# Performance work log

Hardware: AMD Instinct MI355X
Metric: run time of the kernel (lower is better)

## Reference

```python
import jax, jax.numpy as jnp
import numpy as np

B, N, NC = 16, 25200, 80
CONF_THRES = 0.25
IOU_THRES = 0.45
MAX_DET = 300
MAX_WH = 7680.0   # yolov5 per-class box offset for class-aware NMS
TOPK = 1024       # pre-NMS candidate cap (fixed-shape stand-in for yolov5 max_nms)


def setup_inputs():
    key = jax.random.key(0)
    k1, k2 = jax.random.split(key)
    # xywh in pixel units (640x640 image, boxes up to ~120 px); obj/cls confidences in [0,1]
    xywh = jax.random.uniform(k1, (B, N, 4), dtype=jnp.float32) * jnp.array([640.0, 640.0, 120.0, 120.0], jnp.float32)
    conf = jax.random.uniform(k2, (B, N, 1 + NC), dtype=jnp.float32)
    return {"YOLOoutput": jnp.concatenate([xywh, conf], axis=-1)}


def _xywh2xyxy(x):
    cx, cy, w, h = x[..., 0], x[..., 1], x[..., 2], x[..., 3]
    return jnp.stack([cx - w / 2, cy - h / 2, cx + w / 2, cy + h / 2], axis=-1)


def _pairwise_iou(a, b):
    # a, b: [K,4] xyxy -> [K,K]
    lt = jnp.maximum(a[:, None, :2], b[None, :, :2])
    rb = jnp.minimum(a[:, None, 2:], b[None, :, 2:])
    wh = jnp.maximum(rb - lt, 0.0)
    inter = wh[..., 0] * wh[..., 1]
    area_a = (a[:, 2] - a[:, 0]) * (a[:, 3] - a[:, 1])
    area_b = (b[:, 2] - b[:, 0]) * (b[:, 3] - b[:, 1])
    return inter / (area_a[:, None] + area_b[None, :] - inter + 1e-7)


def _nms_single(pred):
    # pred: [N, 5+NC]
    obj = pred[:, 4]
    cls_conf = pred[:, 5:] * obj[:, None]      # conf = obj_conf * cls_conf (yolov5)
    conf = jnp.max(cls_conf, axis=-1)
    j = jnp.argmax(cls_conf, axis=-1)
    valid = (obj > CONF_THRES) & (conf > CONF_THRES)
    box = _xywh2xyxy(pred[:, :4])
    scores = jnp.where(valid, conf, -1.0)      # invalid candidates sink to bottom
    top_scores, idx = jax.lax.top_k(scores, TOPK)
    b = box[idx]                               # [TOPK,4]
    c = j[idx].astype(box.dtype)
    boxes_off = b + (c * MAX_WH)[:, None]      # class-aware NMS via per-class offset
    valid_k = top_scores > 0.0
    iou = _pairwise_iou(boxes_off, boxes_off)
    ar = jnp.arange(TOPK)

    def body(i, supp):
        active = jnp.logical_not(supp[i])
        return supp | (active & (iou[i] > IOU_THRES) & (ar > i))

    supp = jax.lax.fori_loop(0, TOPK, body, jnp.logical_not(valid_k))
    keep = valid_k & jnp.logical_not(supp)
    fs, fi = jax.lax.top_k(jnp.where(keep, top_scores, -1.0), MAX_DET)
    dv = fs > 0.0
    det_box = b[fi] * dv[:, None]              # zero out padded rows
    det = jnp.concatenate(
        [det_box, jnp.where(dv, fs, 0.0)[:, None], (c[fi] * dv)[:, None]], axis=-1
    )                                          # [MAX_DET, 6] = x1,y1,x2,y2,conf,cls
    return det, dv


def reference(YOLOoutput):
    det, dvalid = jax.vmap(_nms_single)(YOLOoutput)   # [B,MAX_DET,6], [B,MAX_DET]
    scores = det[..., 4]
    mean_conf = jnp.max(scores, axis=1)               # = 0 when image has no detections
    n = dvalid.sum(axis=1)
    terms = jnp.abs(det[..., 0:2] - det[..., 2:4]) * scores[..., None]  # padded rows are 0
    s = terms.sum(axis=(1, 2))
    wh = jnp.where(n > 0, s / (2.0 * jnp.maximum(n, 1)), 0.0)  # mean over n*2 elements
    conf_addition = mean_conf.sum() / B
    w_and_h = wh.sum() / B
    return conf_addition, w_and_h, det[2]
```

## Files before the change

kernel.cpp:

```cpp
#include <hip/hip_runtime.h>
#include <hip/hip_bf16.h>

typedef unsigned long long u64;
typedef unsigned int u32;

#define BATCH 16
#define NANCH 25200
#define NCLS 80
#define NFEAT 85
#define TOPK 1024
#define MAXDET 300
#define CONF_T 0.25f
#define IOU_T 0.45f
#define MAX_WH 7680.0f

#define TILE_A 128
#define TILES_PER_BLK 4

__global__ __launch_bounds__(512) void score_kernel(const float* __restrict__ in,
                                                    u64* __restrict__ keys) {
    __shared__ float ld[TILE_A * NFEAT];
    const int b = blockIdx.y, tid = threadIdx.x;
    for (int t = 0; t < TILES_PER_BLK; ++t) {
        const int tile = blockIdx.x * TILES_PER_BLK + t;
        const int a0 = tile * TILE_A;
        if (a0 >= NANCH) break;
        const int na = min(TILE_A, NANCH - a0);
        const int nf4 = na * NFEAT / 4;
        const float4* src = (const float4*)(in + ((size_t)b * NANCH + a0) * NFEAT);
        if (t) __syncthreads();
        for (int k = tid; k < nf4; k += 512) ((float4*)ld)[k] = src[k];
        __syncthreads();
        const int a = tid >> 2, q = tid & 3;
        if (a < na) {
            const float* p = ld + a * NFEAT;
            float obj = p[4];
            float best = -1e30f;
            int bj = 0;
#pragma unroll
            for (int k = 0; k < 20; ++k) {
                float v = p[5 + q * 20 + k] * obj;
                if (v > best) { best = v; bj = q * 20 + k; }
            }
#pragma unroll
            for (int d = 1; d < 4; d <<= 1) {
                float ob = __shfl_xor(best, d, 64);
                int oj = __shfl_xor(bj, d, 64);
                if (ob > best || (ob == best && oj < bj)) { best = ob; bj = oj; }
            }
            if (q == 0) {
                bool valid = (obj > CONF_T) && (best > CONF_T);
                float sc = valid ? best : -1.0f;
                u32 sb = __float_as_uint(sc);
                u32 ord = sb ^ ((sb & 0x80000000u) ? 0xFFFFFFFFu : 0x80000000u);
                int idx = a0 + a;
                keys[(size_t)b * NANCH + idx] =
                    ((u64)ord << 32) | ((u64)((u32)(idx ^ 0xFFFF) & 0xFFFFu) << 8) | (u64)bj;
            }
        }
    }
}

__global__ __launch_bounds__(1024) void select_topk(const u64* __restrict__ keys,
                                                    const float* __restrict__ in,
                                                    float4* __restrict__ box4,
                                                    float4* __restrict__ boxoff4,
                                                    float* __restrict__ score,
                                                    float* __restrict__ cls,
                                                    u64* __restrict__ vmask) {
    const int b = blockIdx.x, tid = threadIdx.x;
    const u64* kb = keys + (size_t)b * NANCH;
    __shared__ u32 hist[256];
    __shared__ u32 sfx[256];
    __shared__ u32 s_prefix, s_cg, s_cnt;
    __shared__ u64 buf[2048];

    if (tid == 0) { s_prefix = 0u; s_cg = 0u; }
    for (int p = 0; p < 4; ++p) {
        if (tid < 256) hist[tid] = 0u;
        __syncthreads();
        const u32 prefix = s_prefix;
        const u32 cg = s_cg;
        const int sh_match = 32 - 8 * p;
        const int sh_dig = 24 - 8 * p;
#pragma unroll 4
        for (int n = tid; n < NANCH; n += 1024) {
            u32 hi = (u32)(kb[n] >> 32);
            if (((u64)(hi ^ prefix) >> sh_match) == 0ull)
                atomicAdd(&hist[(hi >> sh_dig) & 0xFFu], 1u);
        }
        __syncthreads();
        if (tid < 256) sfx[tid] = hist[tid];
        __syncthreads();
        for (int off = 1; off < 256; off <<= 1) {
            u32 v = 0u;
            if (tid < 256 && tid + off < 256) v = sfx[tid + off];
            __syncthreads();
            if (tid < 256) sfx[tid] += v;
            __syncthreads();
        }
        const u32 need = (u32)TOPK - cg;
        if (tid < 256) {
            u32 s0 = sfx[tid];
            u32 s1 = (tid < 255) ? sfx[tid + 1] : 0u;
            if (s0 >= need && s1 < need) {
                s_prefix = prefix | ((u32)tid << sh_dig);
                s_cg = cg + s1;
            }
        }
        __syncthreads();
    }
    const u32 thr = s_prefix;
    if (tid == 0) s_cnt = 0u;
    __syncthreads();
#pragma unroll 4
    for (int n = tid; n < NANCH; n += 1024) {
        u64 k = kb[n];
        if ((u32)(k >> 32) > thr) {
            u32 pos = atomicAdd(&s_cnt, 1u);
            if (pos < 2048u) buf[pos] = k;
        }
    }
    __syncthreads();
#pragma unroll 4
    for (int n = tid; n < NANCH; n += 1024) {
        u64 k = kb[n];
        if ((u32)(k >> 32) == thr) {
            u32 pos = atomicAdd(&s_cnt, 1u);
            if (pos < 2048u) buf[pos] = k;
        }
    }
    __syncthreads();
    u32 cnt = s_cnt; if (cnt > 2048u) cnt = 2048u;
    for (int n = (int)cnt + tid; n < 2048; n += 1024) buf[n] = 0ull;
    __syncthreads();
    for (int k2 = 2; k2 <= 2048; k2 <<= 1) {
        for (int jj = k2 >> 1; jj > 0; jj >>= 1) {
            int i = ((tid & ~(jj - 1)) << 1) | (tid & (jj - 1));
            int part = i | jj;
            u64 a = buf[i], c = buf[part];
            bool sw = ((i & k2) == 0) ? (a < c) : (a > c);
            if (sw) { buf[i] = c; buf[part] = a; }
            __syncthreads();
        }
    }
    u64 k = buf[tid];
    u32 ord = (u32)(k >> 32);
    u32 sb = (ord & 0x80000000u) ? (ord ^ 0x80000000u) : ~ord;
    float sc = __uint_as_float(sb);
    int idx = (int)((((u32)(k >> 8)) & 0xFFFFu) ^ 0xFFFFu);
    int j = (int)(k & 0xFFu);
    const float* pr = in + ((size_t)b * NANCH + idx) * NFEAT;
    float cx = pr[0], cy = pr[1], ww = pr[2], hh = pr[3];
    float x1 = cx - ww / 2.0f, y1 = cy - hh / 2.0f;
    float x2 = cx + ww / 2.0f, y2 = cy + hh / 2.0f;
    float c = (float)j;
    float cm = c * MAX_WH;
    box4[b * TOPK + tid]    = make_float4(x1, y1, x2, y2);
    boxoff4[b * TOPK + tid] = make_float4(x1 + cm, y1 + cm, x2 + cm, y2 + cm);
    score[b * TOPK + tid] = sc;
    cls[b * TOPK + tid] = c;
    u64 bal = __ballot(sc > 0.0f);
    if ((tid & 63) == 0) vmask[b * 16 + (tid >> 6)] = bal;
}

__global__ __launch_bounds__(256) void iou_mask(const float4* __restrict__ boxoff4,
                                                u64* __restrict__ M) {
    const int wavei = (blockIdx.x << 2) | (threadIdx.x >> 6);
    const int lane = threadIdx.x & 63;
    const int b = wavei >> 10;
    const int i = wavei & 1023;
    const float4 A = boxoff4[b * TOPK + i];
    const float areaA = (A.z - A.x) * (A.w - A.y);
    u64 myword = 0ull;
#pragma unroll 4
    for (int t = 0; t < 16; ++t) {
        int j = (t << 6) | lane;
        float4 Bx = boxoff4[b * TOPK + j];
        float lx = fmaxf(A.x, Bx.x), ly = fmaxf(A.y, Bx.y);
        float rx = fminf(A.z, Bx.z), ry = fminf(A.w, Bx.w);
        float iw = fmaxf(rx - lx, 0.0f), ih = fmaxf(ry - ly, 0.0f);
        float inter = iw * ih;
        float areaB = (Bx.z - Bx.x) * (Bx.w - Bx.y);
        float iou = inter / (areaA + areaB - inter + 1e-7f);
        bool pred = (iou > IOU_T) && (j > i);
        u64 bal = __ballot(pred);
        if (lane == t) myword = bal;
    }
    if (lane < 16) M[((size_t)b * 16 + lane) * TOPK + i] = myword;
}

__global__ __launch_bounds__(64) void nms_seq(const u64* __restrict__ M,
                                              const u64* __restrict__ vmask,
                                              u64* __restrict__ keepmask) {
    const int lane = threadIdx.x;
    const int b = blockIdx.x * 4 + (lane >> 4);
    const int w = lane & 15;
    u64 supp = ~vmask[b * 16 + w];
    const u64* Mw = M + ((size_t)b * 16 + w) * TOPK;
    const u64* Mbase = M + (size_t)b * 16 * TOPK;
    for (int wb = 0; wb < 16; ++wb) {
        u64 cur = __shfl(supp, (lane & 48) | wb, 64);
        const u64* Mc = Mbase + (size_t)wb * TOPK;
        u64 rw[8], rc[8], nw[8], nc[8];
#pragma unroll
        for (int q = 0; q < 8; ++q) { rw[q] = Mw[wb * 64 + q]; rc[q] = Mc[wb * 64 + q]; }
        for (int cblk = 0; cblk < 8; ++cblk) {
            if (cblk < 7) {
                const int i0n = wb * 64 + (cblk + 1) * 8;
#pragma unroll
                for (int q = 0; q < 8; ++q) { nw[q] = Mw[i0n + q]; nc[q] = Mc[i0n + q]; }
            }
#pragma unroll
            for (int q = 0; q < 8; ++q) {
                int ii = cblk * 8 + q;
                u64 msk = ((cur >> ii) & 1ull) ? 0ull : ~0ull;
                supp |= rw[q] & msk;
                cur  |= rc[q] & msk;
            }
#pragma unroll
            for (int q = 0; q < 8; ++q) { rw[q] = nw[q]; rc[q] = nc[q]; }
        }
    }
    keepmask[b * 16 + w] = vmask[b * 16 + w] & ~supp;
}

__global__ __launch_bounds__(256) void finalize(const float4* __restrict__ box4,
                                                const float* __restrict__ score,
                                                const float* __restrict__ cls,
                                                const u64* __restrict__ keepmask,
                                                float* __restrict__ out) {
    const int b = blockIdx.x, tid = threadIdx.x;
    __shared__ u64 kw[16];
    __shared__ int wpfx[17];
    __shared__ float sdet[MAXDET * 6];
    __shared__ float s_sum, s_max;
    if (tid < 16) kw[tid] = keepmask[b * 16 + tid];
    if (tid == 0) { s_sum = 0.0f; s_max = 0.0f; }
    __syncthreads();
    if (tid == 0) {
        int acc = 0;
        for (int w = 0; w < 16; ++w) { wpfx[w] = acc; acc += __popcll(kw[w]); }
        wpfx[16] = acc;
    }
    for (int t = tid; t < MAXDET * 6; t += 256) sdet[t] = 0.0f;
    __syncthreads();
    for (int r = tid; r < TOPK; r += 256) {
        int w = r >> 6, bp = r & 63;
        if ((kw[w] >> bp) & 1ull) {
            int pos = wpfx[w] + __popcll(kw[w] & ((1ull << bp) - 1ull));
            if (pos < MAXDET) {
                float4 bx = box4[b * TOPK + r];
                float s = score[b * TOPK + r];
                float c = cls[b * TOPK + r];
                sdet[pos * 6 + 0] = bx.x;
                sdet[pos * 6 + 1] = bx.y;
                sdet[pos * 6 + 2] = bx.z;
                sdet[pos * 6 + 3] = bx.w;
                sdet[pos * 6 + 4] = s;
                sdet[pos * 6 + 5] = c;
                float term = (fabsf(bx.x - bx.z) + fabsf(bx.y - bx.w)) * s;
                atomicAdd(&s_sum, term);
                if (pos == 0) s_max = s;
            }
        }
    }
    __syncthreads();
    if (tid == 0) {
        int n = wpfx[16]; if (n > MAXDET) n = MAXDET;
        float wh = (n > 0) ? (s_sum / (2.0f * (float)n)) : 0.0f;
        atomicAdd(&out[0], s_max / (float)BATCH);
        atomicAdd(&out[1], wh / (float)BATCH);
    }
    if (b == 2) {
        for (int t = tid; t < MAXDET * 6; t += 256) out[2 + t] = sdet[t];
    }
}

extern "C" void kernel_launch(void* const* d_in, const int* in_sizes, int n_in,
                              void* d_out, int out_size, void* d_ws, size_t ws_size,
                              hipStream_t stream) {
    const float* in = (const float*)d_in[0];
    float* out = (float*)d_out;
    char* ws = (char*)d_ws;

    u64*    keys     = (u64*)   (ws + 0);
    float4* boxoff4  = (float4*)(ws + 3225600);
    float4* box4     = (float4*)(ws + 3225600 + 262144);
    float*  score    = (float*) (ws + 3749888);
    float*  cls      = (float*) (ws + 3815424);
    u64*    vmask    = (u64*)   (ws + 3880960);
    u64*    M        = (u64*)   (ws + 3883008);
    u64*    keepmask = (u64*)   (ws + 5980160);

    hipMemsetAsync(out, 0, 2 * sizeof(float), stream);
    score_kernel<<<dim3(50, BATCH), 512, 0, stream>>>(in, keys);
    select_topk<<<BATCH, 1024, 0, stream>>>(keys, in, box4, boxoff4, score, cls, vmask);
    iou_mask<<<BATCH * TOPK / 4, 256, 0, stream>>>(boxoff4, M);
    nms_seq<<<4, 64, 0, stream>>>(M, vmask, keepmask);
    finalize<<<BATCH, 256, 0, stream>>>(box4, score, cls, keepmask, out);
}
```

Before: 341.2 us.

## Use wave shuffles for histogram scan, bitonic sort stages, and transpose NMS mask

The histogram suffix scan in top-k selection becomes a single-wave shuffle scan instead of a barrier-heavy shared-memory loop. The 2048-element bitonic sort keeps each wave's 128 elements in registers and does the substages with jj of 64 or less via shuffles, so only the larger strides go through shared memory with block barriers. The IoU mask is stored row-major ([b][i][word]) so the sequential NMS kernel can read contiguous rows and get the current-word column by shuffling instead of loading it separately. These changes aim to cut __syncthreads counts and improve memory coalescing in the latency-bound serial stages, at the cost of more register pressure.

```diff
diff --git a/kernel.cpp b/kernel.cpp
--- a/kernel.cpp
+++ b/kernel.cpp
@@ -90,15 +90,23 @@
                 atomicAdd(&hist[(hi >> sh_dig) & 0xFFu], 1u);
         }
         __syncthreads();
-        if (tid < 256) sfx[tid] = hist[tid];
-        __syncthreads();
-        for (int off = 1; off < 256; off <<= 1) {
-            u32 v = 0u;
-            if (tid < 256 && tid + off < 256) v = sfx[tid + off];
-            __syncthreads();
-            if (tid < 256) sfx[tid] += v;
-            __syncthreads();
-        }
+        if (tid < 64) {
+            u32 h0 = hist[tid * 4], h1 = hist[tid * 4 + 1];
+            u32 h2 = hist[tid * 4 + 2], h3 = hist[tid * 4 + 3];
+            u32 s3v = h3, s2v = h2 + s3v, s1v = h1 + s2v, s0v = h0 + s1v;
+            u32 S = s0v;
+#pragma unroll
+            for (int d = 1; d < 64; d <<= 1) {
+                u32 o = __shfl_down(S, d, 64);
+                if (tid + d < 64) S += o;
+            }
+            u32 E = S - s0v;
+            sfx[tid * 4]     = E + s0v;
+            sfx[tid * 4 + 1] = E + s1v;
+            sfx[tid * 4 + 2] = E + s2v;
+            sfx[tid * 4 + 3] = E + s3v;
+        }
+        __syncthreads();
         const u32 need = (u32)TOPK - cg;
         if (tid < 256) {
             u32 s0 = sfx[tid];
@@ -134,8 +142,31 @@
     u32 cnt = s_cnt; if (cnt > 2048u) cnt = 2048u;
     for (int n = (int)cnt + tid; n < 2048; n += 1024) buf[n] = 0ull;
     __syncthreads();
-    for (int k2 = 2; k2 <= 2048; k2 <<= 1) {
-        for (int jj = k2 >> 1; jj > 0; jj >>= 1) {
+
+    const int wv = tid >> 6, l = tid & 63;
+    const int base = wv * 128;
+    u64 r0 = buf[base + l], r1 = buf[base + 64 + l];
+    for (int k2 = 2; k2 <= 128; k2 <<= 1) {
+        const bool d0 = (((base + l) & k2) == 0);
+        const bool d1 = (((base + 64 + l) & k2) == 0);
+        for (int jj = (k2 >> 1); jj >= 1; jj >>= 1) {
+            if (jj == 64) {
+                u64 mx = r0 > r1 ? r0 : r1, mn = r0 > r1 ? r1 : r0;
+                r0 = d0 ? mx : mn; r1 = d0 ? mn : mx;
+            } else {
+                const bool up = (l & jj) != 0;
+                u64 v0 = __shfl_xor(r0, jj, 64);
+                u64 v1 = __shfl_xor(r1, jj, 64);
+                const bool km0 = (d0 != up), km1 = (d1 != up);
+                r0 = km0 ? (r0 > v0 ? r0 : v0) : (r0 < v0 ? r0 : v0);
+                r1 = km1 ? (r1 > v1 ? r1 : v1) : (r1 < v1 ? r1 : v1);
+            }
+        }
+    }
+    for (int k2 = 256; k2 <= 2048; k2 <<= 1) {
+        buf[base + l] = r0; buf[base + 64 + l] = r1;
+        __syncthreads();
+        for (int jj = (k2 >> 1); jj >= 128; jj >>= 1) {
             int i = ((tid & ~(jj - 1)) << 1) | (tid & (jj - 1));
             int part = i | jj;
             u64 a = buf[i], c = buf[part];
@@ -143,7 +174,25 @@
             if (sw) { buf[i] = c; buf[part] = a; }
             __syncthreads();
         }
-    }
+        r0 = buf[base + l]; r1 = buf[base + 64 + l];
+        const bool d0 = (((base + l) & k2) == 0);
+        for (int jj = 64; jj >= 1; jj >>= 1) {
+            if (jj == 64) {
+                u64 mx = r0 > r1 ? r0 : r1, mn = r0 > r1 ? r1 : r0;
+                r0 = d0 ? mx : mn; r1 = d0 ? mn : mx;
+            } else {
+                const bool up = (l & jj) != 0;
+                u64 v0 = __shfl_xor(r0, jj, 64);
+                u64 v1 = __shfl_xor(r1, jj, 64);
+                const bool km = (d0 != up);
+                r0 = km ? (r0 > v0 ? r0 : v0) : (r0 < v0 ? r0 : v0);
+                r1 = km ? (r1 > v1 ? r1 : v1) : (r1 < v1 ? r1 : v1);
+            }
+        }
+    }
+    buf[base + l] = r0; buf[base + 64 + l] = r1;
+    __syncthreads();
+
     u64 k = buf[tid];
     u32 ord = (u32)(k >> 32);
     u32 sb = (ord & 0x80000000u) ? (ord ^ 0x80000000u) : ~ord;
@@ -187,7 +236,7 @@
         u64 bal = __ballot(pred);
         if (lane == t) myword = bal;
     }
-    if (lane < 16) M[((size_t)b * 16 + lane) * TOPK + i] = myword;
+    if (lane < 16) M[((size_t)b * TOPK + i) * 16 + lane] = myword;
 }
 
 __global__ __launch_bounds__(64) void nms_seq(const u64* __restrict__ M,
@@ -196,30 +245,33 @@
     const int lane = threadIdx.x;
     const int b = blockIdx.x * 4 + (lane >> 4);
     const int w = lane & 15;
+    const int grp = lane & 48;
     u64 supp = ~vmask[b * 16 + w];
-    const u64* Mw = M + ((size_t)b * 16 + w) * TOPK;
-    const u64* Mbase = M + (size_t)b * 16 * TOPK;
+    const u64* Mb = M + (size_t)b * TOPK * 16;
+    u64 rwA[16], rwB[16];
+#pragma unroll
+    for (int q = 0; q < 16; ++q) rwA[q] = Mb[q * 16 + w];
     for (int wb = 0; wb < 16; ++wb) {
-        u64 cur = __shfl(supp, (lane & 48) | wb, 64);
-        const u64* Mc = Mbase + (size_t)wb * TOPK;
-        u64 rw[8], rc[8], nw[8], nc[8];
-#pragma unroll
-        for (int q = 0; q < 8; ++q) { rw[q] = Mw[wb * 64 + q]; rc[q] = Mc[wb * 64 + q]; }
-        for (int cblk = 0; cblk < 8; ++cblk) {
-            if (cblk < 7) {
-                const int i0n = wb * 64 + (cblk + 1) * 8;
-#pragma unroll
-                for (int q = 0; q < 8; ++q) { nw[q] = Mw[i0n + q]; nc[q] = Mc[i0n + q]; }
-            }
-#pragma unroll
-            for (int q = 0; q < 8; ++q) {
-                int ii = cblk * 8 + q;
-                u64 msk = ((cur >> ii) & 1ull) ? 0ull : ~0ull;
-                supp |= rw[q] & msk;
-                cur  |= rc[q] & msk;
-            }
-#pragma unroll
-            for (int q = 0; q < 8; ++q) { rw[q] = nw[q]; rc[q] = nc[q]; }
+        u64 cur = __shfl(supp, grp | wb, 64);
+#pragma unroll
+        for (int c4 = 0; c4 < 4; ++c4) {
+            const int rn = wb * 64 + (c4 + 1) * 16;
+            if (rn < 1024) {
+#pragma unroll
+                for (int q = 0; q < 16; ++q) rwB[q] = Mb[(rn + q) * 16 + w];
+            }
+            u64 rc[16];
+#pragma unroll
+            for (int q = 0; q < 16; ++q) rc[q] = __shfl(rwA[q], grp | wb, 64);
+#pragma unroll
+            for (int q = 0; q < 16; ++q) {
+                const int ii = c4 * 16 + q;
+                const bool act = ((cur >> ii) & 1ull) == 0ull;
+                supp = act ? (supp | rwA[q]) : supp;
+                cur  = act ? (cur  | rc[q])  : cur;
+            }
+#pragma unroll
+            for (int q = 0; q < 16; ++q) rwA[q] = rwB[q];
         }
     }
     keepmask[b * 16 + w] = vmask[b * 16 + w] & ~supp;
@@ -286,7 +338,7 @@
 
     u64*    keys     = (u64*)   (ws + 0);
     float4* boxoff4  = (float4*)(ws + 3225600);
-    float4* box4     = (float4*)(ws + 3225600 + 262144);
+    float4* box4     = (float4*)(ws + 3487744);
     float*  score    = (float*) (ws + 3749888);
     float*  cls      = (float*) (ws + 3815424);
     u64*    vmask    = (u64*)   (ws + 3880960);
```

Result: faster. 315.4 us (-7.5%).
